# Optimization experiments

Measured on AMD Instinct MI355X. Metric: run time of the kernel, lower is better.

The kernel has to match this reference:

```python
import jax, jax.numpy as jnp
import numpy as np

RESOLUTION = 7
RATIOS = (0.25, 0.125, 0.0625, 0.03125)  # spatial scales for P2..P5
SAMPLE_RATIO = 2
BASE_SIZE = 224.0
BASE_LEVEL = 4.0
LEVEL_MIN = 2.0  # -log2(1/4)
LEVEL_MAX = 5.0  # -log2(1/32)
EPS = 1e-6
IMG = 800.0


def _make_boxes(key, n):
    k1, k2, k3, k4 = jax.random.split(key, 4)
    # log-uniform box sizes in [16, 512] px so rois hit all FPN levels
    w = jnp.exp2(jax.random.uniform(k1, (n,), minval=4.0, maxval=9.0))
    h = jnp.exp2(jax.random.uniform(k2, (n,), minval=4.0, maxval=9.0))
    cx = jax.random.uniform(k3, (n,), minval=0.0, maxval=IMG)
    cy = jax.random.uniform(k4, (n,), minval=0.0, maxval=IMG)
    x1 = jnp.clip(cx - w / 2, 0.0, IMG - 1)
    y1 = jnp.clip(cy - h / 2, 0.0, IMG - 1)
    x2 = jnp.clip(cx + w / 2, 0.0, IMG - 1)
    y2 = jnp.clip(cy + h / 2, 0.0, IMG - 1)
    return jnp.stack([x1, y1, jnp.maximum(x2, x1), jnp.maximum(y2, y1)], axis=1)


def setup_inputs() -> dict:
    key = jax.random.key(0)
    ks = jax.random.split(key, 8)
    N, C = 2, 256
    sizes = [(200, 200), (100, 100), (50, 50), (25, 25), (13, 13)]
    feats = {f"feat{i}": jax.random.normal(ks[i], (N, C, h, w), dtype=jnp.float32)
             for i, (h, w) in enumerate(sizes)}
    feats["props0"] = _make_boxes(ks[5], 512)
    feats["props1"] = _make_boxes(ks[6], 512)
    return feats


def _axis_interp(v, size):
    """Per-axis bilinear setup, matching torchvision RoIAlign (aligned=False)."""
    valid = (v >= -1.0) & (v <= size)
    v0 = jnp.maximum(v, 0.0)
    lo = jnp.floor(v0).astype(jnp.int32)
    at_edge = lo >= size - 1
    lo = jnp.where(at_edge, size - 1, lo)
    hi = jnp.where(at_edge, size - 1, lo + 1)
    frac = jnp.where(at_edge, 0.0, v0 - lo.astype(v.dtype))
    return lo, hi, frac, valid


def _roi_align(feat, rois, scale, res=RESOLUTION, sr=SAMPLE_RATIO):
    """feat: [N,C,H,W], rois: [R,5] (batch_idx,x1,y1,x2,y2) -> [R,C,res,res]."""
    N, C, H, W = feat.shape
    b = rois[:, 0].astype(jnp.int32)
    x1, y1, x2, y2 = (rois[:, 1] * scale, rois[:, 2] * scale,
                      rois[:, 3] * scale, rois[:, 4] * scale)
    roi_w = jnp.maximum(x2 - x1, 1.0)
    roi_h = jnp.maximum(y2 - y1, 1.0)
    bin_w = roi_w / res
    bin_h = roi_h / res
    P = res * sr
    offs = (jnp.arange(P, dtype=jnp.float32) + 0.5) / sr  # sample offsets in bin units
    ys = y1[:, None] + offs[None, :] * bin_h[:, None]  # [R,P]
    xs = x1[:, None] + offs[None, :] * bin_w[:, None]  # [R,P]
    yl, yh, fy, vy = _axis_interp(ys, H)
    xl, xh, fx, vx = _axis_interp(xs, W)
    bi = b[:, None, None]

    def g(yi, xi):  # gather corner values -> [R,P,P,C]
        return feat[bi, :, yi[:, :, None], xi[:, None, :]]

    hy, hx = 1.0 - fy, 1.0 - fx
    val = (g(yl, xl) * (hy[:, :, None] * hx[:, None, :])[..., None]
           + g(yl, xh) * (hy[:, :, None] * fx[:, None, :])[..., None]
           + g(yh, xl) * (fy[:, :, None] * hx[:, None, :])[..., None]
           + g(yh, xh) * (fy[:, :, None] * fx[:, None, :])[..., None])
    val = jnp.where((vy[:, :, None] & vx[:, None, :])[..., None], val, 0.0)
    R = rois.shape[0]
    pooled = val.reshape(R, res, sr, res, sr, C).mean(axis=(2, 4))  # [R,res,res,C]
    return pooled.transpose(0, 3, 1, 2)


def _pool(features, proposals):
    # convert: concat proposals with batch indices -> rois [R,5]
    inds = jnp.concatenate([jnp.full((p.shape[0], 1), i, dtype=p.dtype)
                            for i, p in enumerate(proposals)], axis=0)
    boxes = jnp.concatenate(proposals, axis=0)
    rois = jnp.concatenate([inds, boxes], axis=1)
    rois = jax.lax.stop_gradient(rois)  # torchvision RoIAlign has no roi grad
    # set_level: FPN level assignment (eq.1 of FPN paper)
    areas = (rois[:, 3] - rois[:, 1] + 1) * (rois[:, 4] - rois[:, 2] + 1)
    sizes = jnp.sqrt(areas)
    levels = jnp.floor(BASE_LEVEL + jnp.log2(sizes / BASE_SIZE + EPS))
    levels = (jnp.clip(levels, LEVEL_MIN, LEVEL_MAX) - LEVEL_MIN).astype(jnp.int32)
    R, C = rois.shape[0], features[0].shape[1]
    results = jnp.zeros((R, C, RESOLUTION, RESOLUTION), dtype=boxes.dtype)
    for lvl in range(len(RATIOS)):  # forward uses features[:-1]
        pooled = _roi_align(features[lvl], rois, RATIOS[lvl])
        results = results + jnp.where((levels == lvl)[:, None, None, None], pooled, 0.0)
    return results


def reference(feat0, feat1, feat2, feat3, feat4, props0, props1):
    return _pool([feat0, feat1, feat2, feat3, feat4], [props0, props1])
```

## Files before the change

### kernel.cpp

```cpp
#include <hip/hip_runtime.h>
#include <math.h>

#define C_CH 256
#define RESO 7
#define NBIN 49

__device__ __forceinline__ unsigned short f2bf(float f) {
  unsigned int u = __float_as_uint(f);
  u = (u + 0x7fffu + ((u >> 16) & 1u)) >> 16;
  return (unsigned short)u;
}
__device__ __forceinline__ float bf_lo(unsigned int u) { return __uint_as_float(u << 16); }
__device__ __forceinline__ float bf_hi(unsigned int u) { return __uint_as_float(u & 0xffff0000u); }

struct TArgs {
  const float* src[4];
  unsigned short* dst[4];
  int hw[4];
  int bx0[5];
};

__global__ __launch_bounds__(256) void conv_nhwc_bf16(TArgs a) {
  __shared__ float tile[64][65];
  const int bx = blockIdx.x;
  int l = 0;
  if (bx >= a.bx0[1]) l = 1;
  if (bx >= a.bx0[2]) l = 2;
  if (bx >= a.bx0[3]) l = 3;
  const int HW = a.hw[l];
  const int hw0 = (bx - a.bx0[l]) * 64;
  const int c0 = blockIdx.y * 64;
  const int n = blockIdx.z;

  const float* s = a.src[l] + (size_t)n * C_CH * HW;
  unsigned short* d = a.dst[l] + (size_t)n * HW * C_CH;

  const int t = threadIdx.x;
  const int lane16 = t & 15;
  const int row16 = t >> 4;

  if (hw0 + 64 <= HW && (HW & 3) == 0) {
    float4 v[4];
#pragma unroll
    for (int i = 0; i < 4; ++i) {
      const int c_l = row16 + 16 * i;
      v[i] = *(const float4*)(s + (size_t)(c0 + c_l) * HW + hw0 + lane16 * 4);
    }
#pragma unroll
    for (int i = 0; i < 4; ++i) {
      const int c_l = row16 + 16 * i;
      tile[c_l][lane16 * 4 + 0] = v[i].x;
      tile[c_l][lane16 * 4 + 1] = v[i].y;
      tile[c_l][lane16 * 4 + 2] = v[i].z;
      tile[c_l][lane16 * 4 + 3] = v[i].w;
    }
  } else {
    for (int i = 0; i < 4; ++i) {
      const int c_l = row16 + 16 * i;
      const float* row = s + (size_t)(c0 + c_l) * HW;
      for (int k = 0; k < 4; ++k) {
        const int hw = hw0 + lane16 * 4 + k;
        tile[c_l][lane16 * 4 + k] = (hw < HW) ? row[hw] : 0.0f;
      }
    }
  }
  __syncthreads();

#pragma unroll
  for (int i = 0; i < 4; ++i) {
    const int hw_l = row16 + 16 * i;
    const int hww = hw0 + hw_l;
    if (hww < HW) {
      const int c4 = lane16 * 4;
      const unsigned int lo = (unsigned int)f2bf(tile[c4 + 0][hw_l]) |
                              ((unsigned int)f2bf(tile[c4 + 1][hw_l]) << 16);
      const unsigned int hi = (unsigned int)f2bf(tile[c4 + 2][hw_l]) |
                              ((unsigned int)f2bf(tile[c4 + 3][hw_l]) << 16);
      *(uint2*)(d + (size_t)hww * C_CH + c0 + c4) = make_uint2(lo, hi);
    }
  }
}

__global__ __launch_bounds__(512) void roi_gather_bf16(
    const unsigned short* __restrict__ f0, const unsigned short* __restrict__ f1,
    const unsigned short* __restrict__ f2, const unsigned short* __restrict__ f3,
    const float* __restrict__ props0, const float* __restrict__ props1,
    float* __restrict__ out) {
  __shared__ float obuf[NBIN * C_CH];
  __shared__ int s_o0[2][14], s_o1[2][14];
  __shared__ float s_w0[2][14], s_w1[2][14];

  const int r = blockIdx.x;
  const int t = threadIdx.x;
  const int b = (r >= 512) ? 1 : 0;
  const float* pr = (b ? props1 : props0) + (r & 511) * 4;
  const float x1 = pr[0], y1 = pr[1], x2 = pr[2], y2 = pr[3];

  const float size = sqrtf((x2 - x1 + 1.0f) * (y2 - y1 + 1.0f));
  float lv = floorf(4.0f + log2f(size / 224.0f + 1e-6f));
  lv = fminf(fmaxf(lv, 2.0f), 5.0f) - 2.0f;
  const int lvl = (int)lv;

  const int Htab[4] = {200, 100, 50, 25};
  const float stab[4] = {0.25f, 0.125f, 0.0625f, 0.03125f};
  const int H = Htab[lvl];
  const int W = H;
  const float sc = stab[lvl];
  const unsigned short* fl = (lvl == 0) ? f0 : (lvl == 1) ? f1 : (lvl == 2) ? f2 : f3;

  const float rx1 = x1 * sc, ry1 = y1 * sc;
  const float roi_w = fmaxf(x2 * sc - rx1, 1.0f);
  const float roi_h = fmaxf(y2 * sc - ry1, 1.0f);
  const float bw = roi_w / 7.0f, bh = roi_h / 7.0f;

  if (t < 28) {
    const int axis = t / 14;
    const int k = t % 14;
    const float off = ((float)k + 0.5f) * 0.5f;
    const float v = axis ? (rx1 + off * bw) : (ry1 + off * bh);
    const int isz = H;
    const bool valid = (v >= -1.0f) && (v <= (float)isz);
    const float v0 = fmaxf(v, 0.0f);
    int lo = (int)floorf(v0);
    const bool edge = (lo >= isz - 1);
    lo = edge ? isz - 1 : lo;
    const int hi = edge ? isz - 1 : lo + 1;
    const float fr = edge ? 0.0f : (v0 - (float)lo);
    const int mul = axis ? C_CH : W * C_CH;
    s_o0[axis][k] = lo * mul;
    s_o1[axis][k] = hi * mul;
    s_w1[axis][k] = valid ? fr : 0.0f;
    s_w0[axis][k] = valid ? (1.0f - fr) : 0.0f;
  }
  __syncthreads();

  const int wv = t >> 6;
  const int ln = t & 63;
  const int cg = ln & 31;
  const int xt = ln >> 5;
  const size_t HWp = (size_t)H * W;
  const unsigned short* base = fl + (size_t)b * HWp * C_CH + cg * 8;

  for (int bb = wv; bb < NBIN; bb += 8) {
    const int ph = bb / 7, pw = bb - ph * 7;
    float acc[8] = {0.f, 0.f, 0.f, 0.f, 0.f, 0.f, 0.f, 0.f};
#pragma unroll
    for (int s1 = 0; s1 < 2; ++s1) {
      const int sy = 2 * ph + s1;
      const int yo0 = s_o0[0][sy], yo1 = s_o1[0][sy];
      const float wy0 = s_w0[0][sy], wy1 = s_w1[0][sy];
#pragma unroll
      for (int s2 = 0; s2 < 2; ++s2) {
        const int sx = 2 * pw + s2;
        const int xo = xt ? s_o1[1][sx] : s_o0[1][sx];
        const float wx = xt ? s_w1[1][sx] : s_w0[1][sx];
        const uint4 q0 = *(const uint4*)(base + yo0 + xo);
        const uint4 q1 = *(const uint4*)(base + yo1 + xo);
        const float w0 = wx * wy0, w1 = wx * wy1;
        acc[0] += w0 * bf_lo(q0.x) + w1 * bf_lo(q1.x);
        acc[1] += w0 * bf_hi(q0.x) + w1 * bf_hi(q1.x);
        acc[2] += w0 * bf_lo(q0.y) + w1 * bf_lo(q1.y);
        acc[3] += w0 * bf_hi(q0.y) + w1 * bf_hi(q1.y);
        acc[4] += w0 * bf_lo(q0.z) + w1 * bf_lo(q1.z);
        acc[5] += w0 * bf_hi(q0.z) + w1 * bf_hi(q1.z);
        acc[6] += w0 * bf_lo(q0.w) + w1 * bf_lo(q1.w);
        acc[7] += w0 * bf_hi(q0.w) + w1 * bf_hi(q1.w);
      }
    }
#pragma unroll
    for (int k = 0; k < 8; ++k) acc[k] += __shfl_xor(acc[k], 32);
    const int cbase = cg * 8 + xt * 4;
#pragma unroll
    for (int k = 0; k < 4; ++k)
      obuf[(cbase + k) * NBIN + bb] = acc[xt * 4 + k] * 0.25f;
  }
  __syncthreads();

  float4* o4 = (float4*)(out + (size_t)r * (NBIN * C_CH));
  const float4* ob4 = (const float4*)obuf;
  for (int i = t; i < NBIN * C_CH / 4; i += 512) o4[i] = ob4[i];
}

__global__ __launch_bounds__(256) void roi_gather_nchw(
    const float* __restrict__ f0, const float* __restrict__ f1,
    const float* __restrict__ f2, const float* __restrict__ f3,
    const float* __restrict__ props0, const float* __restrict__ props1,
    float* __restrict__ out) {
  __shared__ float obuf[NBIN * C_CH];
  __shared__ int s_o0[2][14], s_o1[2][14];
  __shared__ float s_w0[2][14], s_w1[2][14];

  const int r = blockIdx.x;
  const int t = threadIdx.x;
  const int b = (r >= 512) ? 1 : 0;
  const float* pr = (b ? props1 : props0) + (r & 511) * 4;
  const float x1 = pr[0], y1 = pr[1], x2 = pr[2], y2 = pr[3];
  const float size = sqrtf((x2 - x1 + 1.0f) * (y2 - y1 + 1.0f));
  float lv = floorf(4.0f + log2f(size / 224.0f + 1e-6f));
  lv = fminf(fmaxf(lv, 2.0f), 5.0f) - 2.0f;
  const int lvl = (int)lv;
  const int Htab[4] = {200, 100, 50, 25};
  const float stab[4] = {0.25f, 0.125f, 0.0625f, 0.03125f};
  const int H = Htab[lvl];
  const int W = H;
  const float sc = stab[lvl];
  const float* fl = (lvl == 0) ? f0 : (lvl == 1) ? f1 : (lvl == 2) ? f2 : f3;
  const float rx1 = x1 * sc, ry1 = y1 * sc;
  const float roi_w = fmaxf(x2 * sc - rx1, 1.0f);
  const float roi_h = fmaxf(y2 * sc - ry1, 1.0f);
  const float bw = roi_w / 7.0f, bh = roi_h / 7.0f;
  if (t < 28) {
    const int axis = t / 14;
    const int k = t % 14;
    const float off = ((float)k + 0.5f) * 0.5f;
    const float v = axis ? (rx1 + off * bw) : (ry1 + off * bh);
    const int isz = H;
    const bool valid = (v >= -1.0f) && (v <= (float)isz);
    const float v0 = fmaxf(v, 0.0f);
    int lo = (int)floorf(v0);
    const bool edge = (lo >= isz - 1);
    lo = edge ? isz - 1 : lo;
    const int hi = edge ? isz - 1 : lo + 1;
    const float fr = edge ? 0.0f : (v0 - (float)lo);
    const int mul = axis ? 1 : W;
    s_o0[axis][k] = lo * mul;
    s_o1[axis][k] = hi * mul;
    s_w1[axis][k] = valid ? fr : 0.0f;
    s_w0[axis][k] = valid ? (1.0f - fr) : 0.0f;
  }
  __syncthreads();
  const int wv = t >> 6;
  const int ln = t & 63;
  const size_t HWp = (size_t)H * W;
  const float* base = fl + ((size_t)b * C_CH + ln * 4) * HWp;
  for (int bb = wv; bb < NBIN; bb += 4) {
    const int ph = bb / 7, pw = bb - ph * 7;
    float4 acc = make_float4(0.f, 0.f, 0.f, 0.f);
    for (int s1 = 0; s1 < 2; ++s1) {
      const int sy = 2 * ph + s1;
      const int yo0 = s_o0[0][sy], yo1 = s_o1[0][sy];
      const float wy0 = s_w0[0][sy], wy1 = s_w1[0][sy];
      for (int s2 = 0; s2 < 2; ++s2) {
        const int sx = 2 * pw + s2;
        const int xo0 = s_o0[1][sx], xo1 = s_o1[1][sx];
        const float w00 = wy0 * s_w0[1][sx], w01 = wy0 * s_w1[1][sx];
        const float w10 = wy1 * s_w0[1][sx], w11 = wy1 * s_w1[1][sx];
        float e[4];
        for (int j = 0; j < 4; ++j) {
          e[j] = w00 * base[j * HWp + yo0 + xo0] + w01 * base[j * HWp + yo0 + xo1] +
                 w10 * base[j * HWp + yo1 + xo0] + w11 * base[j * HWp + yo1 + xo1];
        }
        acc.x += e[0]; acc.y += e[1]; acc.z += e[2]; acc.w += e[3];
      }
    }
    const int c4 = ln * 4;
    obuf[(c4 + 0) * NBIN + bb] = acc.x * 0.25f;
    obuf[(c4 + 1) * NBIN + bb] = acc.y * 0.25f;
    obuf[(c4 + 2) * NBIN + bb] = acc.z * 0.25f;
    obuf[(c4 + 3) * NBIN + bb] = acc.w * 0.25f;
  }
  __syncthreads();
  float4* o4 = (float4*)(out + (size_t)r * (NBIN * C_CH));
  const float4* ob4 = (const float4*)obuf;
  for (int i = t; i < NBIN * C_CH / 4; i += 256) o4[i] = ob4[i];
}

extern "C" void kernel_launch(void* const* d_in, const int* in_sizes, int n_in,
                              void* d_out, int out_size, void* d_ws, size_t ws_size,
                              hipStream_t stream) {
  const float* f0 = (const float*)d_in[0];
  const float* f1 = (const float*)d_in[1];
  const float* f2 = (const float*)d_in[2];
  const float* f3 = (const float*)d_in[3];
  const float* p0 = (const float*)d_in[5];
  const float* p1 = (const float*)d_in[6];
  float* out = (float*)d_out;
  unsigned short* ws = (unsigned short*)d_ws;

  const int HWs[4] = {200 * 200, 100 * 100, 50 * 50, 25 * 25};
  size_t off[4];
  size_t acc = 0;
  for (int l = 0; l < 4; ++l) {
    off[l] = acc;
    acc += (size_t)2 * C_CH * HWs[l];
  }
  const size_t need_bytes = acc * sizeof(unsigned short);

  if (ws_size >= need_bytes) {
    TArgs a;
    a.src[0] = f0; a.src[1] = f1; a.src[2] = f2; a.src[3] = f3;
    int cum = 0;
    for (int l = 0; l < 4; ++l) {
      a.dst[l] = ws + off[l];
      a.hw[l] = HWs[l];
      a.bx0[l] = cum;
      cum += (HWs[l] + 63) / 64;
    }
    a.bx0[4] = cum;
    dim3 grid(cum, 4, 2);
    dim3 block(256);
    conv_nhwc_bf16<<<grid, block, 0, stream>>>(a);
    roi_gather_bf16<<<1024, 512, 0, stream>>>(a.dst[0], a.dst[1], a.dst[2], a.dst[3],
                                              p0, p1, out);
  } else {
    roi_gather_nchw<<<1024, 256, 0, stream>>>(f0, f1, f2, f3, p0, p1, out);
  }
}
```

Baseline: 200.5 us.

## Make NHWC bf16 conversion persistent with prefetched tiles and nontemporal memory ops

The NCHW-to-NHWC bf16 transpose kernel becomes a grid-stride persistent kernel capped at 2048 blocks. Each block prefetches the next tile into registers while it converts and writes the current one. Input loads and the ROI output stores now use nontemporal builtins so streaming data does not pollute the cache. The trade-off is more register use and an extra barrier per tile, and the nontemporal hints may behave differently on this hardware.

```diff
diff --git a/kernel.cpp b/kernel.cpp
--- a/kernel.cpp
+++ b/kernel.cpp
@@ -4,6 +4,9 @@
 #define C_CH 256
 #define RESO 7
 #define NBIN 49
+
+typedef float fx4 __attribute__((ext_vector_type(4)));
+typedef unsigned int ux2 __attribute__((ext_vector_type(2)));
 
 __device__ __forceinline__ unsigned short f2bf(float f) {
   unsigned int u = __float_as_uint(f);
@@ -17,67 +20,107 @@
   const float* src[4];
   unsigned short* dst[4];
   int hw[4];
-  int bx0[5];
+  int tilesx[4];
+  int tbase[5];
+  int total;
 };
+
+__device__ __forceinline__ void decode_tile(const TArgs& a, int T, int& l, int& hw0,
+                                            int& c0, int& n, int& HW) {
+  int ll = 0;
+  if (T >= a.tbase[1]) ll = 1;
+  if (T >= a.tbase[2]) ll = 2;
+  if (T >= a.tbase[3]) ll = 3;
+  const int idx = T - a.tbase[ll];
+  const int txs = a.tilesx[ll];
+  const int tx = idx % txs;
+  const int rem = idx / txs;
+  l = ll;
+  hw0 = tx * 64;
+  c0 = (rem & 3) * 64;
+  n = rem >> 2;
+  HW = a.hw[ll];
+}
+
+__device__ __forceinline__ void load_tile(const TArgs& a, int l, int hw0, int c0, int n,
+                                          int HW, int lane16, int row16, fx4 v[4]) {
+  const float* s = a.src[l] + (size_t)n * C_CH * HW;
+  if (((HW & 3) == 0) && (hw0 + 64 <= HW)) {
+#pragma unroll
+    for (int i = 0; i < 4; ++i) {
+      const int c_l = row16 + 16 * i;
+      v[i] = __builtin_nontemporal_load(
+          (const fx4*)(s + (size_t)(c0 + c_l) * HW + hw0 + lane16 * 4));
+    }
+  } else {
+#pragma unroll
+    for (int i = 0; i < 4; ++i) {
+      const int c_l = row16 + 16 * i;
+      const float* row = s + (size_t)(c0 + c_l) * HW;
+#pragma unroll
+      for (int k = 0; k < 4; ++k) {
+        const int hw = hw0 + lane16 * 4 + k;
+        v[i][k] = (hw < HW) ? row[hw] : 0.0f;
+      }
+    }
+  }
+}
 
 __global__ __launch_bounds__(256) void conv_nhwc_bf16(TArgs a) {
   __shared__ float tile[64][65];
-  const int bx = blockIdx.x;
-  int l = 0;
-  if (bx >= a.bx0[1]) l = 1;
-  if (bx >= a.bx0[2]) l = 2;
-  if (bx >= a.bx0[3]) l = 3;
-  const int HW = a.hw[l];
-  const int hw0 = (bx - a.bx0[l]) * 64;
-  const int c0 = blockIdx.y * 64;
-  const int n = blockIdx.z;
-
-  const float* s = a.src[l] + (size_t)n * C_CH * HW;
-  unsigned short* d = a.dst[l] + (size_t)n * HW * C_CH;
-
   const int t = threadIdx.x;
   const int lane16 = t & 15;
   const int row16 = t >> 4;
-
-  if (hw0 + 64 <= HW && (HW & 3) == 0) {
-    float4 v[4];
+  const int stride = gridDim.x;
+
+  int T = blockIdx.x;
+  int l0, hw00, c00, n0, HW0;
+  decode_tile(a, T, l0, hw00, c00, n0, HW0);
+  fx4 v[4];
+  load_tile(a, l0, hw00, c00, n0, HW0, lane16, row16, v);
+
+  while (true) {
+    __syncthreads();
 #pragma unroll
     for (int i = 0; i < 4; ++i) {
       const int c_l = row16 + 16 * i;
-      v[i] = *(const float4*)(s + (size_t)(c0 + c_l) * HW + hw0 + lane16 * 4);
-    }
+      tile[c_l][lane16 * 4 + 0] = v[i][0];
+      tile[c_l][lane16 * 4 + 1] = v[i][1];
+      tile[c_l][lane16 * 4 + 2] = v[i][2];
+      tile[c_l][lane16 * 4 + 3] = v[i][3];
+    }
+
+    const int Tn = T + stride;
+    const bool more = Tn < a.total;
+    int l1, hw01, c01, n1, HW1;
+    fx4 w[4];
+    if (more) {
+      decode_tile(a, Tn, l1, hw01, c01, n1, HW1);
+      load_tile(a, l1, hw01, c01, n1, HW1, lane16, row16, w);
+    }
+    __syncthreads();
+
+    unsigned short* d = a.dst[l0] + (size_t)n0 * HW0 * C_CH;
 #pragma unroll
     for (int i = 0; i < 4; ++i) {
-      const int c_l = row16 + 16 * i;
-      tile[c_l][lane16 * 4 + 0] = v[i].x;
-      tile[c_l][lane16 * 4 + 1] = v[i].y;
-      tile[c_l][lane16 * 4 + 2] = v[i].z;
-      tile[c_l][lane16 * 4 + 3] = v[i].w;
-    }
-  } else {
-    for (int i = 0; i < 4; ++i) {
-      const int c_l = row16 + 16 * i;
-      const float* row = s + (size_t)(c0 + c_l) * HW;
-      for (int k = 0; k < 4; ++k) {
-        const int hw = hw0 + lane16 * 4 + k;
-        tile[c_l][lane16 * 4 + k] = (hw < HW) ? row[hw] : 0.0f;
+      const int hw_l = row16 + 16 * i;
+      const int hww = hw00 + hw_l;
+      if (hww < HW0) {
+        const int c4 = lane16 * 4;
+        ux2 p;
+        p.x = (unsigned int)f2bf(tile[c4 + 0][hw_l]) |
+              ((unsigned int)f2bf(tile[c4 + 1][hw_l]) << 16);
+        p.y = (unsigned int)f2bf(tile[c4 + 2][hw_l]) |
+              ((unsigned int)f2bf(tile[c4 + 3][hw_l]) << 16);
+        *(ux2*)(d + (size_t)hww * C_CH + c00 + c4) = p;
       }
     }
-  }
-  __syncthreads();
-
-#pragma unroll
-  for (int i = 0; i < 4; ++i) {
-    const int hw_l = row16 + 16 * i;
-    const int hww = hw0 + hw_l;
-    if (hww < HW) {
-      const int c4 = lane16 * 4;
-      const unsigned int lo = (unsigned int)f2bf(tile[c4 + 0][hw_l]) |
-                              ((unsigned int)f2bf(tile[c4 + 1][hw_l]) << 16);
-      const unsigned int hi = (unsigned int)f2bf(tile[c4 + 2][hw_l]) |
-                              ((unsigned int)f2bf(tile[c4 + 3][hw_l]) << 16);
-      *(uint2*)(d + (size_t)hww * C_CH + c0 + c4) = make_uint2(lo, hi);
-    }
+
+    if (!more) break;
+    T = Tn;
+    l0 = l1; hw00 = hw01; c00 = c01; n0 = n1; HW0 = HW1;
+#pragma unroll
+    for (int i = 0; i < 4; ++i) v[i] = w[i];
   }
 }
 
@@ -176,9 +219,10 @@
   }
   __syncthreads();
 
-  float4* o4 = (float4*)(out + (size_t)r * (NBIN * C_CH));
-  const float4* ob4 = (const float4*)obuf;
-  for (int i = t; i < NBIN * C_CH / 4; i += 512) o4[i] = ob4[i];
+  fx4* o4 = (fx4*)(out + (size_t)r * (NBIN * C_CH));
+  const fx4* ob4 = (const fx4*)obuf;
+  for (int i = t; i < NBIN * C_CH / 4; i += 512)
+    __builtin_nontemporal_store(ob4[i], o4 + i);
 }
 
 __global__ __launch_bounds__(256) void roi_gather_nchw(
@@ -293,13 +337,14 @@
     for (int l = 0; l < 4; ++l) {
       a.dst[l] = ws + off[l];
       a.hw[l] = HWs[l];
-      a.bx0[l] = cum;
-      cum += (HWs[l] + 63) / 64;
-    }
-    a.bx0[4] = cum;
-    dim3 grid(cum, 4, 2);
-    dim3 block(256);
-    conv_nhwc_bf16<<<grid, block, 0, stream>>>(a);
+      a.tilesx[l] = (HWs[l] + 63) / 64;
+      a.tbase[l] = cum;
+      cum += a.tilesx[l] * 4 * 2;
+    }
+    a.tbase[4] = cum;
+    a.total = cum;
+    const int nblocks = (cum < 2048) ? cum : 2048;
+    conv_nhwc_bf16<<<nblocks, 256, 0, stream>>>(a);
     roi_gather_bf16<<<1024, 512, 0, stream>>>(a.dst[0], a.dst[1], a.dst[2], a.dst[3],
                                               p0, p1, out);
   } else {
```

After: 188.5 us. 6.0% less time.
